# Performance work log

Measured on AMD Instinct MI355X. Metric: run time of the kernel, lower is better.

## Reference

```python
import jax, jax.numpy as jnp
import numpy as np

B, LH, HF = 65536, 128, 32
VC_MIN = 0.0


def _theta_init():
    # Deterministic parameter init, matching the torch constructor defaults.
    def spinv(x):
        return float(np.log(np.exp(max(x, 1e-4)) - 1.0 + 1e-6))
    vals = [
        0.0,                                  # alpha_raw: log(0.5/(1-0.5))
        float(np.log(np.exp(1.0) - 1.0 + 1e-6)),   # c_raw  (c_init=1.0)
        float(np.log(np.exp(0.1) - 1.0 + 1e-6)),   # kappa_raw (kappa_init=0.1)
        float(np.log(np.exp(0.15) - 1.0 + 1e-6)),  # vc_raw (vc_eff=0.15)
        -6.0,   # log_qx
        -6.0,   # log_qu
        -5.0,   # log_r
        0.0,    # log_q_scale
        -6.0,   # log_p0_xx
        -4.0,   # log_p0_uu
        spinv(0.1),   # a1_raw
        spinv(0.05),  # d1_raw
        spinv(0.5),   # d2_raw
        spinv(0.5),   # d3_raw
        0.0,    # b1
        0.0,    # b2
        0.1,    # beta
        float(np.arctanh(0.9)),  # rho_m_raw
        -4.0,   # log_qm
        -4.0,   # log_p0_mm
    ]
    return np.asarray(vals, dtype=np.float32)


def setup_inputs() -> dict:
    key = jax.random.key(0)
    k1, k2, k3, k4, k5 = jax.random.split(key, 5)
    return {
        "v_hist": jax.random.normal(k1, (B, LH), dtype=jnp.float32),
        "dt_hist": 0.01 + 0.1 * jax.random.uniform(k2, (B, LH), dtype=jnp.float32),
        "x_obs_hist": jax.random.normal(k3, (B, LH), dtype=jnp.float32),
        "v_fut": jax.random.normal(k4, (B, HF), dtype=jnp.float32),
        "dt_fut": 0.01 + 0.1 * jax.random.uniform(k5, (B, HF), dtype=jnp.float32),
        "theta": jnp.asarray(_theta_init()),
    }


def _forward(v_hist, dt_hist, x_obs_hist, v_fut, dt_fut, theta):
    sp = jax.nn.softplus
    alpha = jax.nn.sigmoid(theta[0])
    c = sp(theta[1]); kappa = sp(theta[2]); vc = sp(theta[3]) + VC_MIN
    qx = jnp.exp(theta[4]); qu = jnp.exp(theta[5]); R = jnp.exp(theta[6])
    qs = jnp.exp(theta[7]); p0xx = jnp.exp(theta[8]); p0uu = jnp.exp(theta[9])
    a1 = sp(theta[10]); d1 = sp(theta[11]); d2 = sp(theta[12]); d3 = sp(theta[13])
    b1 = theta[14]; b2 = theta[15]; beta = theta[16]
    rho_m = jnp.tanh(theta[17]); qm = jnp.exp(theta[18]); p0mm = jnp.exp(theta[19])

    Bn, Lh = v_hist.shape
    dtype = v_hist.dtype
    eye = jnp.eye(3, dtype=dtype)

    def predict(s, P, v, dv, dt):
        x, u, m = s[:, 0], s[:, 1], s[:, 2]
        rho = jnp.exp(-alpha * dt)
        forcing = jax.nn.relu(v * v - vc * vc)
        cl = (-a1 * u + b1 * v + b2 * dv
              - d1 * u * u - d2 * u * jnp.abs(v) - d3 * u * jnp.abs(u))
        x_p = x + u * dt
        u_p = rho * u - kappa * x * dt + c * forcing * dt + cl * dt + beta * m
        m_p = rho_m * m
        s_p = jnp.stack([x_p, u_p, m_p], axis=1)
        z = jnp.zeros_like(dt); o = jnp.ones_like(dt)
        Fm = jnp.stack([
            jnp.stack([o, dt, z], axis=1),
            jnp.stack([-kappa * dt, rho, beta * o], axis=1),
            jnp.stack([z, z, rho_m * o], axis=1)], axis=1)  # [B,3,3]
        qdiag = jnp.stack([qs * qx * dt, qs * qu * dt, qm * o], axis=1)  # [B,3]
        P_p = jnp.einsum('bij,bjk,blk->bil', Fm, P, Fm) + qdiag[:, :, None] * eye
        return s_p, P_p

    def update(s, P, y):
        innov = y - s[:, 0]
        S = P[:, 0, 0] + R
        K = P[:, :, 0] / S[:, None]            # [B,3]
        s_u = s + K * innov[:, None]
        IKH = eye - K[:, :, None] * eye[0]     # I - K H, H = [1,0,0]
        P_u = (jnp.einsum('bij,bjk,blk->bil', IKH, P, IKH)
               + R * (K[:, :, None] * K[:, None, :]))
        return s_u, P_u

    s0 = jnp.zeros((Bn, 3), dtype).at[:, 0].set(x_obs_hist[:, 0])
    P0 = jnp.broadcast_to(jnp.diag(jnp.stack([p0xx, p0uu, p0mm])).astype(dtype),
                          (Bn, 3, 3))

    # History steps k = 1 .. Lh-1 (scan over time axis, [T, B] layout)
    v_h = v_hist[:, :Lh - 1].T
    dv_h = jnp.concatenate(
        [jnp.zeros((1, Bn), dtype), (v_hist[:, 1:Lh - 1] - v_hist[:, :Lh - 2]).T], axis=0)
    dt_h = jnp.maximum(dt_hist[:, 1:], 1e-6).T
    y_h = x_obs_hist[:, 1:].T

    def hist_step(carry, inp):
        s, P = carry
        v, dv, dt, y = inp
        s, P = predict(s, P, v, dv, dt)
        s, P = update(s, P, y)
        return (s, P), None

    (s, P), _ = jax.lax.scan(hist_step, (s0, P0), (v_h, dv_h, dt_h, y_h))

    # Future rollout (predict only)
    v_f = v_fut.T
    dv_f = (v_fut - jnp.concatenate([v_hist[:, -1:], v_fut[:, :-1]], axis=1)).T
    dt_f = jnp.maximum(dt_fut, 1e-6).T

    def fut_step(carry, inp):
        s, P = carry
        v, dv, dt = inp
        s, P = predict(s, P, v, dv, dt)
        return (s, P), (s[:, 0], P[:, 0, 0], s[:, 1])

    _, (x_preds, x_vars, u_ests) = jax.lax.scan(fut_step, (s, P), (v_f, dv_f, dt_f))
    return x_preds.T, x_vars.T, u_ests.T  # each [B, Hf]


def reference(v_hist, dt_hist, x_obs_hist, v_fut, dt_fut, theta):
    return _forward(v_hist, dt_hist, x_obs_hist, v_fut, dt_fut, theta)
```

## Files before the change

### kernel.cpp

```cpp
#include <hip/hip_runtime.h>
#include <math.h>

#define BATCH 65536
#define LHIST 128
#define HFUT  32

__device__ __forceinline__ float softplusf(float x) {
    return fmaxf(x, 0.0f) + log1pf(expf(-fabsf(x)));
}

__global__ __launch_bounds__(256, 1) void kalman_fwd(
    const float* __restrict__ v_hist,
    const float* __restrict__ dt_hist,
    const float* __restrict__ x_obs,
    const float* __restrict__ v_fut,
    const float* __restrict__ dt_fut,
    const float* __restrict__ theta,
    float* __restrict__ out)
{
    const int b = blockIdx.x * blockDim.x + threadIdx.x;

    const float alpha = 1.0f / (1.0f + expf(-theta[0]));
    const float c     = softplusf(theta[1]);
    const float kappa = softplusf(theta[2]);
    const float vc    = softplusf(theta[3]);
    const float qx    = expf(theta[4]);
    const float qu    = expf(theta[5]);
    const float Rn    = expf(theta[6]);
    const float qs    = expf(theta[7]);
    const float p0xx  = expf(theta[8]);
    const float p0uu  = expf(theta[9]);
    const float a1    = softplusf(theta[10]);
    const float d1    = softplusf(theta[11]);
    const float d2    = softplusf(theta[12]);
    const float d3    = softplusf(theta[13]);
    const float b1    = theta[14];
    const float b2    = theta[15];
    const float beta  = theta[16];
    const float rho_m = tanhf(theta[17]);
    const float qm    = expf(theta[18]);
    const float p0mm  = expf(theta[19]);
    const float vc2   = vc * vc;
    const float qxs   = qs * qx;
    const float qus   = qs * qu;

    float sx = 0.0f, su = 0.0f, sm = 0.0f;
    float p00 = p0xx, p01 = 0.0f, p02 = 0.0f, p11 = p0uu, p12 = 0.0f, p22 = p0mm;

    auto predict = [&](float v, float dv, float dt_raw) {
        float dt  = fmaxf(dt_raw, 1e-6f);
        float rho = expf(-alpha * dt);
        float forcing = fmaxf(v * v - vc2, 0.0f);
        float cl = -a1 * su + b1 * v + b2 * dv
                 - d1 * su * su - d2 * su * fabsf(v) - d3 * su * fabsf(su);
        float kdt = kappa * dt;
        float x_p = sx + su * dt;
        float u_p = rho * su - kdt * sx + c * forcing * dt + cl * dt + beta * sm;
        float m_p = rho_m * sm;
        float f0 = p00 + dt * p01;
        float f1 = p01 + dt * p11;
        float f2 = p02 + dt * p12;
        float g0 = -kdt * p00 + rho * p01 + beta * p02;
        float g1 = -kdt * p01 + rho * p11 + beta * p12;
        float g2 = -kdt * p02 + rho * p12 + beta * p22;
        float n00 = f0 + dt * f1 + qxs * dt;
        float n01 = -kdt * f0 + rho * f1 + beta * f2;
        float n02 = rho_m * f2;
        float n11 = -kdt * g0 + rho * g1 + beta * g2 + qus * dt;
        float n12 = rho_m * g2;
        float n22 = rho_m * rho_m * p22 + qm;
        sx = x_p; su = u_p; sm = m_p;
        p00 = n00; p01 = n01; p02 = n02; p11 = n11; p12 = n12; p22 = n22;
    };

    auto update = [&](float y) {
        float innov = y - sx;
        float S    = p00 + Rn;
        float Sinv = __builtin_amdgcn_rcpf(S);
        float K0 = p00 * Sinv, K1 = p01 * Sinv, K2 = p02 * Sinv;
        sx += K0 * innov; su += K1 * innov; sm += K2 * innov;
        float a = 1.0f - K0;
        float n00 = a * a * p00 + Rn * K0 * K0;
        float n01 = a * (p01 - K1 * p00) + Rn * K0 * K1;
        float n02 = a * (p02 - K2 * p00) + Rn * K0 * K2;
        float n11 = S * K1 * K1 - 2.0f * K1 * p01 + p11;
        float n12 = S * K1 * K2 - K2 * p01 - K1 * p02 + p12;
        float n22 = S * K2 * K2 - 2.0f * K2 * p02 + p22;
        p00 = n00; p01 = n01; p02 = n02; p11 = n11; p12 = n12; p22 = n22;
    };

    const float4* v4  = (const float4*)(v_hist  + (size_t)b * LHIST);
    const float4* d4  = (const float4*)(dt_hist + (size_t)b * LHIST);
    const float4* y4  = (const float4*)(x_obs   + (size_t)b * LHIST);
    const float4* vf4 = (const float4*)(v_fut   + (size_t)b * HFUT);
    const float4* df4 = (const float4*)(dt_fut  + (size_t)b * HFUT);

    float vf[HFUT], df[HFUT];
    {
        float4* VF = (float4*)vf; float4* DF = (float4*)df;
        #pragma unroll
        for (int i = 0; i < HFUT / 4; ++i) { VF[i] = vf4[i]; DF[i] = df4[i]; }
    }

    float v_bridge = 0.0f, dv_bridge = 0.0f;

    #pragma unroll 1
    for (int k = 0; k < 4; ++k) {
        float vv[32], dd[32], yy[32];
        float4* V = (float4*)vv; float4* D = (float4*)dd; float4* Y = (float4*)yy;
        #pragma unroll
        for (int i = 0; i < 8; ++i) {
            V[i] = v4[8 * k + i];
            D[i] = d4[8 * k + i];
            Y[i] = y4[8 * k + i];
        }
        if (k == 0) {
            sx = yy[0];
            predict(vv[0], 0.0f, dd[1]); update(yy[1]);
        } else {
            predict(v_bridge, dv_bridge, dd[0]); update(yy[0]);
            predict(vv[0], vv[0] - v_bridge, dd[1]); update(yy[1]);
        }
        #pragma unroll
        for (int i = 1; i < 31; ++i) {
            predict(vv[i], vv[i] - vv[i - 1], dd[i + 1]); update(yy[i + 1]);
        }
        v_bridge  = vv[31];
        dv_bridge = vv[31] - vv[30];
    }

    float oxp[HFUT], oxv[HFUT], oue[HFUT];
    float vp = v_bridge;
    #pragma unroll
    for (int j = 0; j < HFUT; ++j) {
        predict(vf[j], vf[j] - vp, df[j]);
        vp = vf[j];
        oxp[j] = sx; oxv[j] = p00; oue[j] = su;
    }

    float4* xp = (float4*)(out + (size_t)b * HFUT);
    float4* xv = (float4*)(out + (size_t)BATCH * HFUT + (size_t)b * HFUT);
    float4* ue = (float4*)(out + 2 * (size_t)BATCH * HFUT + (size_t)b * HFUT);
    float4* OXP = (float4*)oxp; float4* OXV = (float4*)oxv; float4* OUE = (float4*)oue;
    #pragma unroll
    for (int i = 0; i < HFUT / 4; ++i) {
        xp[i] = OXP[i]; xv[i] = OXV[i]; ue[i] = OUE[i];
    }
}

extern "C" void kernel_launch(void* const* d_in, const int* in_sizes, int n_in,
                              void* d_out, int out_size, void* d_ws, size_t ws_size,
                              hipStream_t stream) {
    const float* v_hist  = (const float*)d_in[0];
    const float* dt_hist = (const float*)d_in[1];
    const float* x_obs   = (const float*)d_in[2];
    const float* v_fut   = (const float*)d_in[3];
    const float* dt_fut  = (const float*)d_in[4];
    const float* theta   = (const float*)d_in[5];
    float* out = (float*)d_out;

    dim3 grid(BATCH / 256), block(256);
    hipLaunchKernelGGL(kalman_fwd, grid, block, 0, stream,
                       v_hist, dt_hist, x_obs, v_fut, dt_fut, theta, out);
}
```

Baseline: 186.9 us.

## Double-buffer history loads in 16-step chunks and use native exp2

The history loop now works in 16-step chunks and prefetches the next chunk into a second register buffer while the current chunk is filtered, so global load latency overlaps the serial Kalman recurrence. The future-input loads move to after the history loop. expf(-alpha*dt) is replaced with the hardware exp2 intrinsic using a precomputed -alpha*log2(e), which shortens the predict step. The cost is more live registers for the double buffer and slightly lower exp accuracy.

```diff
diff --git a/kernel.cpp b/kernel.cpp
--- a/kernel.cpp
+++ b/kernel.cpp
@@ -4,6 +4,7 @@
 #define BATCH 65536
 #define LHIST 128
 #define HFUT  32
+#define CH    16
 
 __device__ __forceinline__ float softplusf(float x) {
     return fmaxf(x, 0.0f) + log1pf(expf(-fabsf(x)));
@@ -43,13 +44,14 @@
     const float vc2   = vc * vc;
     const float qxs   = qs * qx;
     const float qus   = qs * qu;
+    const float nal2e = -alpha * 1.44269504088896340736f;
 
     float sx = 0.0f, su = 0.0f, sm = 0.0f;
     float p00 = p0xx, p01 = 0.0f, p02 = 0.0f, p11 = p0uu, p12 = 0.0f, p22 = p0mm;
 
     auto predict = [&](float v, float dv, float dt_raw) {
         float dt  = fmaxf(dt_raw, 1e-6f);
-        float rho = expf(-alpha * dt);
+        float rho = __builtin_amdgcn_exp2f(nal2e * dt);
         float forcing = fmaxf(v * v - vc2, 0.0f);
         float cl = -a1 * su + b1 * v + b2 * dv
                  - d1 * su * su - d2 * su * fabsf(v) - d3 * su * fabsf(su);
@@ -92,41 +94,54 @@
     const float4* v4  = (const float4*)(v_hist  + (size_t)b * LHIST);
     const float4* d4  = (const float4*)(dt_hist + (size_t)b * LHIST);
     const float4* y4  = (const float4*)(x_obs   + (size_t)b * LHIST);
-    const float4* vf4 = (const float4*)(v_fut   + (size_t)b * HFUT);
-    const float4* df4 = (const float4*)(dt_fut  + (size_t)b * HFUT);
 
+    float cv[CH], cd[CH], cy[CH];
+    float nv[CH], nd[CH], ny[CH];
+
+    auto load_chunk = [&](float (&vv)[CH], float (&dd)[CH], float (&yy)[CH], int k) {
+        float4* V = (float4*)vv; float4* D = (float4*)dd; float4* Y = (float4*)yy;
+        #pragma unroll
+        for (int i = 0; i < CH / 4; ++i) {
+            V[i] = v4[(CH / 4) * k + i];
+            D[i] = d4[(CH / 4) * k + i];
+            Y[i] = y4[(CH / 4) * k + i];
+        }
+    };
+
+    load_chunk(cv, cd, cy, 0);
+    load_chunk(nv, nd, ny, 1);
+
+    sx = cy[0];
+    predict(cv[0], 0.0f, cd[1]); update(cy[1]);
+    #pragma unroll
+    for (int i = 1; i < CH - 1; ++i) {
+        predict(cv[i], cv[i] - cv[i - 1], cd[i + 1]); update(cy[i + 1]);
+    }
+    float v_bridge  = cv[CH - 1];
+    float dv_bridge = cv[CH - 1] - cv[CH - 2];
+
+    #pragma unroll 1
+    for (int k = 1; k < LHIST / CH; ++k) {
+        #pragma unroll
+        for (int i = 0; i < CH; ++i) { cv[i] = nv[i]; cd[i] = nd[i]; cy[i] = ny[i]; }
+        if (k < LHIST / CH - 1) load_chunk(nv, nd, ny, k + 1);
+        predict(v_bridge, dv_bridge, cd[0]); update(cy[0]);
+        predict(cv[0], cv[0] - v_bridge, cd[1]); update(cy[1]);
+        #pragma unroll
+        for (int i = 1; i < CH - 1; ++i) {
+            predict(cv[i], cv[i] - cv[i - 1], cd[i + 1]); update(cy[i + 1]);
+        }
+        v_bridge  = cv[CH - 1];
+        dv_bridge = cv[CH - 1] - cv[CH - 2];
+    }
+
+    const float4* vf4 = (const float4*)(v_fut  + (size_t)b * HFUT);
+    const float4* df4 = (const float4*)(dt_fut + (size_t)b * HFUT);
     float vf[HFUT], df[HFUT];
     {
         float4* VF = (float4*)vf; float4* DF = (float4*)df;
         #pragma unroll
         for (int i = 0; i < HFUT / 4; ++i) { VF[i] = vf4[i]; DF[i] = df4[i]; }
-    }
-
-    float v_bridge = 0.0f, dv_bridge = 0.0f;
-
-    #pragma unroll 1
-    for (int k = 0; k < 4; ++k) {
-        float vv[32], dd[32], yy[32];
-        float4* V = (float4*)vv; float4* D = (float4*)dd; float4* Y = (float4*)yy;
-        #pragma unroll
-        for (int i = 0; i < 8; ++i) {
-            V[i] = v4[8 * k + i];
-            D[i] = d4[8 * k + i];
-            Y[i] = y4[8 * k + i];
-        }
-        if (k == 0) {
-            sx = yy[0];
-            predict(vv[0], 0.0f, dd[1]); update(yy[1]);
-        } else {
-            predict(v_bridge, dv_bridge, dd[0]); update(yy[0]);
-            predict(vv[0], vv[0] - v_bridge, dd[1]); update(yy[1]);
-        }
-        #pragma unroll
-        for (int i = 1; i < 31; ++i) {
-            predict(vv[i], vv[i] - vv[i - 1], dd[i + 1]); update(yy[i + 1]);
-        }
-        v_bridge  = vv[31];
-        dv_bridge = vv[31] - vv[30];
     }
 
     float oxp[HFUT], oxv[HFUT], oue[HFUT];
```

Result: faster. 162.2 us (-13.2%).

## Stage history inputs through double-buffered LDS with coalesced cooperative loads

Applied to the files above, without the earlier changes.

Replaces per-thread strided float4 reads of each row's history with cooperative loads where pairs of threads read adjacent float4s of a row, transposed into a double-buffered shared-memory tile of 8 timesteps. Global loads for chunk k+2 are issued while chunk k is being computed. Outputs are staged through shared memory rather than per-thread register arrays. The decay exp is also switched to a native exp2 intrinsic. This trades added LDS traffic and a barrier per chunk for better coalescing and lower register pressure. The output writes remain per-thread strided float4 stores.

```diff
diff --git a/kernel.cpp b/kernel.cpp
--- a/kernel.cpp
+++ b/kernel.cpp
@@ -1,9 +1,11 @@
 #include <hip/hip_runtime.h>
 #include <math.h>
 
-#define BATCH 65536
-#define LHIST 128
-#define HFUT  32
+#define BATCH  65536
+#define LHIST  128
+#define HFUT   32
+#define CH     8
+#define NCHUNK (LHIST / CH)
 
 __device__ __forceinline__ float softplusf(float x) {
     return fmaxf(x, 0.0f) + log1pf(expf(-fabsf(x)));
@@ -18,7 +20,12 @@
     const float* __restrict__ theta,
     float* __restrict__ out)
 {
-    const int b = blockIdx.x * blockDim.x + threadIdx.x;
+    __shared__ float lin[2][3][CH][256];
+    __shared__ float lout[3][HFUT][256];
+
+    const int tid = threadIdx.x;
+    const int b   = blockIdx.x * 256 + tid;
+    const int R0  = blockIdx.x * 256;
 
     const float alpha = 1.0f / (1.0f + expf(-theta[0]));
     const float c     = softplusf(theta[1]);
@@ -43,13 +50,14 @@
     const float vc2   = vc * vc;
     const float qxs   = qs * qx;
     const float qus   = qs * qu;
+    const float nal2e = -alpha * 1.44269504088896340736f;
 
     float sx = 0.0f, su = 0.0f, sm = 0.0f;
     float p00 = p0xx, p01 = 0.0f, p02 = 0.0f, p11 = p0uu, p12 = 0.0f, p22 = p0mm;
 
     auto predict = [&](float v, float dv, float dt_raw) {
         float dt  = fmaxf(dt_raw, 1e-6f);
-        float rho = expf(-alpha * dt);
+        float rho = __builtin_amdgcn_exp2f(nal2e * dt);
         float forcing = fmaxf(v * v - vc2, 0.0f);
         float cl = -a1 * su + b1 * v + b2 * dv
                  - d1 * su * su - d2 * su * fabsf(v) - d3 * su * fabsf(su);
@@ -89,62 +97,102 @@
         p00 = n00; p01 = n01; p02 = n02; p11 = n11; p12 = n12; p22 = n22;
     };
 
-    const float4* v4  = (const float4*)(v_hist  + (size_t)b * LHIST);
-    const float4* d4  = (const float4*)(dt_hist + (size_t)b * LHIST);
-    const float4* y4  = (const float4*)(x_obs   + (size_t)b * LHIST);
-    const float4* vf4 = (const float4*)(v_fut   + (size_t)b * HFUT);
-    const float4* df4 = (const float4*)(dt_fut  + (size_t)b * HFUT);
-
-    float vf[HFUT], df[HFUT];
-    {
-        float4* VF = (float4*)vf; float4* DF = (float4*)df;
-        #pragma unroll
-        for (int i = 0; i < HFUT / 4; ++i) { VF[i] = vf4[i]; DF[i] = df4[i]; }
-    }
-
-    float v_bridge = 0.0f, dv_bridge = 0.0f;
-
-    #pragma unroll 1
-    for (int k = 0; k < 4; ++k) {
-        float vv[32], dd[32], yy[32];
-        float4* V = (float4*)vv; float4* D = (float4*)dd; float4* Y = (float4*)yy;
-        #pragma unroll
-        for (int i = 0; i < 8; ++i) {
-            V[i] = v4[8 * k + i];
-            D[i] = d4[8 * k + i];
-            Y[i] = y4[8 * k + i];
+    const float4* v4g = (const float4*)v_hist;
+    const float4* d4g = (const float4*)dt_hist;
+    const float4* y4g = (const float4*)x_obs;
+    const int q  = tid & 1;
+    const int wA = tid >> 1;
+    const int wB = wA + 128;
+    const size_t rA = (size_t)(R0 + wA) * (LHIST / 4);
+    const size_t rB = (size_t)(R0 + wB) * (LHIST / 4);
+
+    float4 gv0, gv1, gd0, gd1, gy0, gy1;
+
+    auto gload = [&](int k) {
+        const size_t col = 2 * k + q;
+        gv0 = v4g[rA + col];  gv1 = v4g[rB + col];
+        gd0 = d4g[rA + col];  gd1 = d4g[rB + col];
+        gy0 = y4g[rA + col];  gy1 = y4g[rB + col];
+    };
+    auto lwrite = [&](int buf) {
+        const int c0 = 4 * q;
+        #pragma unroll
+        for (int j = 0; j < 4; ++j) {
+            lin[buf][0][c0 + j][wA] = (&gv0.x)[j];
+            lin[buf][0][c0 + j][wB] = (&gv1.x)[j];
+            lin[buf][1][c0 + j][wA] = (&gd0.x)[j];
+            lin[buf][1][c0 + j][wB] = (&gd1.x)[j];
+            lin[buf][2][c0 + j][wA] = (&gy0.x)[j];
+            lin[buf][2][c0 + j][wB] = (&gy1.x)[j];
+        }
+    };
+
+    gload(0); lwrite(0);
+    gload(1);
+    __syncthreads();
+
+    float vp1 = 0.0f, vp2 = 0.0f;
+
+    #pragma unroll 2
+    for (int k = 0; k < NCHUNK; ++k) {
+        const int buf = k & 1;
+        if (k + 1 < NCHUNK) lwrite(buf ^ 1);
+        if (k + 2 < NCHUNK) gload(k + 2);
+
+        float vv[CH], dd[CH], yy[CH];
+        #pragma unroll
+        for (int i = 0; i < CH; ++i) {
+            vv[i] = lin[buf][0][i][tid];
+            dd[i] = lin[buf][1][i][tid];
+            yy[i] = lin[buf][2][i][tid];
         }
         if (k == 0) {
             sx = yy[0];
             predict(vv[0], 0.0f, dd[1]); update(yy[1]);
         } else {
-            predict(v_bridge, dv_bridge, dd[0]); update(yy[0]);
-            predict(vv[0], vv[0] - v_bridge, dd[1]); update(yy[1]);
-        }
-        #pragma unroll
-        for (int i = 1; i < 31; ++i) {
+            predict(vp1, vp1 - vp2, dd[0]); update(yy[0]);
+            predict(vv[0], vv[0] - vp1, dd[1]); update(yy[1]);
+        }
+        #pragma unroll
+        for (int i = 1; i <= CH - 2; ++i) {
             predict(vv[i], vv[i] - vv[i - 1], dd[i + 1]); update(yy[i + 1]);
         }
-        v_bridge  = vv[31];
-        dv_bridge = vv[31] - vv[30];
-    }
-
-    float oxp[HFUT], oxv[HFUT], oue[HFUT];
-    float vp = v_bridge;
+        vp2 = vv[CH - 2]; vp1 = vv[CH - 1];
+        __syncthreads();
+    }
+
+    const float4* vf4 = (const float4*)(v_fut  + (size_t)b * HFUT);
+    const float4* df4 = (const float4*)(dt_fut + (size_t)b * HFUT);
+    float vfl[HFUT], dfl[HFUT];
+    {
+        float4* VF = (float4*)vfl; float4* DF = (float4*)dfl;
+        #pragma unroll
+        for (int i = 0; i < HFUT / 4; ++i) { VF[i] = vf4[i]; DF[i] = df4[i]; }
+    }
+
+    float vp = vp1;
     #pragma unroll
     for (int j = 0; j < HFUT; ++j) {
-        predict(vf[j], vf[j] - vp, df[j]);
-        vp = vf[j];
-        oxp[j] = sx; oxv[j] = p00; oue[j] = su;
+        predict(vfl[j], vfl[j] - vp, dfl[j]);
+        vp = vfl[j];
+        lout[0][j][tid] = sx;
+        lout[1][j][tid] = p00;
+        lout[2][j][tid] = su;
     }
 
     float4* xp = (float4*)(out + (size_t)b * HFUT);
     float4* xv = (float4*)(out + (size_t)BATCH * HFUT + (size_t)b * HFUT);
     float4* ue = (float4*)(out + 2 * (size_t)BATCH * HFUT + (size_t)b * HFUT);
-    float4* OXP = (float4*)oxp; float4* OXV = (float4*)oxv; float4* OUE = (float4*)oue;
     #pragma unroll
-    for (int i = 0; i < HFUT / 4; ++i) {
-        xp[i] = OXP[i]; xv[i] = OXV[i]; ue[i] = OUE[i];
+    for (int q8 = 0; q8 < HFUT / 4; ++q8) {
+        float4 o0, o1, o2;
+        #pragma unroll
+        for (int j = 0; j < 4; ++j) {
+            (&o0.x)[j] = lout[0][4 * q8 + j][tid];
+            (&o1.x)[j] = lout[1][4 * q8 + j][tid];
+            (&o2.x)[j] = lout[2][4 * q8 + j][tid];
+        }
+        xp[q8] = o0; xv[q8] = o1; ue[q8] = o2;
     }
 }
 
```

After: 183.7 us. No clear change (-1.7%).
